# Kernel optimization log

Hardware: AMD Instinct MI355X
Metric: run time of the kernel (lower is better)

Reference implementation:

```python
import jax, jax.numpy as jnp
import numpy as np

N_NODES = 50000
N_EDGES = 800000
NUM_GRAPHS = 128

def _sage_conv(x, src, dst, Wl, b, Wr):
    # PyG SAGEConv: lin_l(mean_{j in N(i)} x_j) + lin_r(x_i); bias only on lin_l
    msgs = x[src]                                             # [E, d] gather
    agg = jax.ops.segment_sum(msgs, dst, num_segments=N_NODES)
    deg = jax.ops.segment_sum(jnp.ones((src.shape[0],), x.dtype), dst,
                              num_segments=N_NODES)
    mean = agg / jnp.maximum(deg, 1.0)[:, None]               # [N, d]
    return mean @ Wl.T + b + x @ Wr.T

def setup_inputs() -> dict:
    key = jax.random.key(0)
    ks = jax.random.split(key, 12)
    d_in, d_h, d_out = 96, 96, 64
    def w(k, o, i):
        return jax.random.normal(k, (o, i), jnp.float32) * (1.0 / np.sqrt(i))
    return {
        "x": jax.random.normal(ks[0], (N_NODES, d_in), jnp.float32),
        "edge_index": jax.random.randint(ks[1], (2, N_EDGES), 0, N_NODES, jnp.int32),
        "batch": jnp.sort(jax.random.randint(ks[2], (N_NODES,), 0, NUM_GRAPHS, jnp.int32)),
        "Wl0": w(ks[3], d_h, d_in), "b0": jnp.zeros((d_h,), jnp.float32), "Wr0": w(ks[4], d_h, d_in),
        "Wl1": w(ks[5], d_h, d_h),  "b1": jnp.zeros((d_h,), jnp.float32), "Wr1": w(ks[6], d_h, d_h),
        "Wl2": w(ks[7], d_out, d_h), "b2": jnp.zeros((d_out,), jnp.float32), "Wr2": w(ks[8], d_out, d_h),
    }

def reference(x, edge_index, batch, Wl0, b0, Wr0, Wl1, b1, Wr1, Wl2, b2, Wr2):
    src, dst = edge_index[0], edge_index[1]
    h = jax.nn.relu(_sage_conv(x, src, dst, Wl0, b0, Wr0))   # dropout: eval mode -> identity
    h = jax.nn.relu(_sage_conv(h, src, dst, Wl1, b1, Wr1))
    h = _sage_conv(h, src, dst, Wl2, b2, Wr2)                 # [N, out]
    # global_mean_pool over graphs
    pooled = jax.ops.segment_sum(h, batch, num_segments=NUM_GRAPHS)
    cnt = jax.ops.segment_sum(jnp.ones((h.shape[0],), h.dtype), batch,
                              num_segments=NUM_GRAPHS)
    return pooled / jnp.maximum(cnt, 1.0)[:, None]            # [num_graphs, out]
```

## Files before the change

kernel.cpp:

```cpp
#include <hip/hip_runtime.h>
#include <stdint.h>
#include <stddef.h>

#define NN 50000
#define NP 50048
#define NE 800000
#define NG 128

#define NBKT 256
#define NPB 196
#define BCAP 4096
#define TILE_E 1536
#define PARTB 521
#define AGB 3125
#define TFB 782

typedef __attribute__((ext_vector_type(8))) short bf16x8;
typedef __attribute__((ext_vector_type(4))) float f32x4;
typedef __attribute__((ext_vector_type(4))) unsigned int u32x4;
typedef unsigned short ushort_t;
typedef unsigned int uint_t;

static __device__ inline ushort_t f2b(float f) {
    union { float f; uint_t u; } v; v.f = f;
    uint_t r = v.u + 0x7FFFu + ((v.u >> 16) & 1u);
    return (ushort_t)(r >> 16);
}
static __device__ inline float blo(uint_t u) {
    union { uint_t u; float f; } v; v.u = u << 16; return v.f;
}
static __device__ inline float bhi(uint_t u) {
    union { uint_t u; float f; } v; v.u = u & 0xFFFF0000u; return v.f;
}

__launch_bounds__(256) static __global__
void part_zero_kernel(const int* __restrict__ src, const int* __restrict__ dst,
                      int* __restrict__ bucket_cnt, uint_t* __restrict__ part,
                      float* __restrict__ out, const int* __restrict__ batch,
                      float* __restrict__ inv_cnt) {
    __shared__ int hist[NBKT];
    int tid = threadIdx.x;
    if (blockIdx.x < PARTB) {
        hist[tid] = 0;
        __syncthreads();
        int base = blockIdx.x * TILE_E;
        int end = min(base + TILE_E, NE);
        for (int i = base + tid; i < end; i += 256)
            atomicAdd(&hist[dst[i] / NPB], 1);
        __syncthreads();
        int r = atomicAdd(&bucket_cnt[tid], hist[tid]);
        __syncthreads();
        hist[tid] = r;
        __syncthreads();
        for (int i = base + tid; i < end; i += 256) {
            int s = src[i], d = dst[i];
            int b = d / NPB;
            int dl = d - b * NPB;
            int p = atomicAdd(&hist[b], 1);
            part[b * BCAP + p] = ((uint_t)dl << 16) | (uint_t)s;
        }
    } else {
        int gid = (blockIdx.x - PARTB) * 256 + tid;
        if (gid < NG * 64) out[gid] = 0.f;
        if (gid < NG) {
            int g = gid;
            int lo = 0, hi = NN;
            while (lo < hi) { int m = (lo + hi) >> 1; if (batch[m] < g) lo = m + 1; else hi = m; }
            int start = lo;
            hi = NN;
            while (lo < hi) { int m = (lo + hi) >> 1; if (batch[m] < g + 1) lo = m + 1; else hi = m; }
            inv_cnt[g] = 1.f / (float)max(lo - start, 1);
        }
    }
}

static __device__ void csr_build_body(int b, char* smem, const uint_t* __restrict__ part,
                                      const int* __restrict__ bucket_cnt,
                                      uint_t* __restrict__ od, ushort_t* __restrict__ csr) {
    uint_t* stage = (uint_t*)smem;
    ushort_t* cstage = (ushort_t*)(smem + 16384);
    int* cnt_s = (int*)(smem + 24576);
    int* scan_l = (int*)(smem + 25600);
    int* cur_l = (int*)(smem + 26624);
    int tid = threadIdx.x;
    int bc = bucket_cnt[tid];
    cnt_s[tid] = bc;
    scan_l[tid] = bc;
    __syncthreads();
    for (int off = 1; off < NBKT; off <<= 1) {
        int t = (tid >= off) ? scan_l[tid - off] : 0;
        __syncthreads();
        scan_l[tid] += t;
        __syncthreads();
    }
    int base = scan_l[b] - cnt_s[b];
    int n = cnt_s[b];
    __syncthreads();
    cnt_s[tid] = 0;
    __syncthreads();
    for (int i = tid; i < n; i += 256) {
        uint_t e = part[(size_t)b * BCAP + i];
        stage[i] = e;
        atomicAdd(&cnt_s[e >> 16], 1);
    }
    __syncthreads();
    int v = cnt_s[tid];
    scan_l[tid] = v;
    __syncthreads();
    for (int off = 1; off < NBKT; off <<= 1) {
        int t = (tid >= off) ? scan_l[tid - off] : 0;
        __syncthreads();
        scan_l[tid] += t;
        __syncthreads();
    }
    int ex = scan_l[tid] - v;
    scan_l[tid] = ex;
    cur_l[tid] = 0;
    __syncthreads();
    int g = b * NPB + tid;
    if (tid < NPB && g < NN) od[g] = ((uint_t)(base + ex) << 8) | (uint_t)v;
    for (int i = tid; i < n; i += 256) {
        uint_t e = stage[i];
        int dl = e >> 16;
        int p = atomicAdd(&cur_l[dl], 1);
        cstage[scan_l[dl] + p] = (ushort_t)(e & 0xFFFFu);
    }
    __syncthreads();
    for (int i = tid; i < n; i += 256) csr[base + i] = cstage[i];
}

template <int DOUT, int NT>
static __device__ void mfma_store(int bid, char* smem, bf16x8 a0, bf16x8 a1, bf16x8 a2,
                                  const float* __restrict__ Wl, const float* __restrict__ bias,
                                  const float* __restrict__ Wr,
                                  ushort_t* __restrict__ tlc, ushort_t* __restrict__ trc) {
    constexpr int DIN = 96;
    short* w_s = (short*)smem;
    int tid = threadIdx.x;
    for (int idx = tid; idx < NT * 3 * 64; idx += 256) {
        int ci = idx >> 6, ln = idx & 63;
        int t = ci / 3, s = ci - 3 * t;
        int o = t * 16 + (ln & 15);
        int c0 = s * 32 + (ln >> 4) * 8;
        const float* wrow = (o < DOUT) ? (Wl + (size_t)o * DIN)
                                       : (Wr + (size_t)(o - DOUT) * DIN);
        float4 v0 = *(const float4*)(wrow + c0);
        float4 v1 = *(const float4*)(wrow + c0 + 4);
        bf16x8 pk;
        pk[0] = (short)f2b(v0.x); pk[1] = (short)f2b(v0.y);
        pk[2] = (short)f2b(v0.z); pk[3] = (short)f2b(v0.w);
        pk[4] = (short)f2b(v1.x); pk[5] = (short)f2b(v1.y);
        pk[6] = (short)f2b(v1.z); pk[7] = (short)f2b(v1.w);
        *(bf16x8*)&w_s[idx * 8] = pk;
    }
    __syncthreads();
    int lane = tid & 63;
    int m0 = bid * 64 + (tid >> 6) * 16;
    const bf16x8* wp = (const bf16x8*)w_s + lane;
    f32x4 acc[NT];
#pragma unroll
    for (int t = 0; t < NT; t++) {
        acc[t] = (f32x4){0.f, 0.f, 0.f, 0.f};
        acc[t] = __builtin_amdgcn_mfma_f32_16x16x32_bf16(a0, wp[(t * 3 + 0) * 64], acc[t], 0, 0, 0);
        acc[t] = __builtin_amdgcn_mfma_f32_16x16x32_bf16(a1, wp[(t * 3 + 1) * 64], acc[t], 0, 0, 0);
        acc[t] = __builtin_amdgcn_mfma_f32_16x16x32_bf16(a2, wp[(t * 3 + 2) * 64], acc[t], 0, 0, 0);
    }
    int quad = lane >> 4, col = lane & 15;
#pragma unroll
    for (int t = 0; t < NT; t++) {
        int o = t * 16 + col;
        bool is_r = (o >= DOUT);
        float bv = is_r ? bias[o - DOUT] : 0.f;
        ushort_t* outp = is_r ? trc : tlc;
        int oo = is_r ? (o - DOUT) : o;
        int cch = oo >> 5, f = oo & 31;
        ushort_t* ob = outp + ((size_t)cch * NN) * 32 + f;
#pragma unroll
        for (int r = 0; r < 4; r++) {
            int node = m0 + quad * 4 + r;
            if (node < NN) ob[(size_t)node * 32] = f2b(acc[t][r] + bv);
        }
    }
}

__launch_bounds__(256) static __global__
void csr_tf0_kernel(const uint_t* __restrict__ part, const int* __restrict__ bucket_cnt,
                    uint_t* __restrict__ od, ushort_t* __restrict__ csr,
                    const float* __restrict__ x, const float* __restrict__ Wl0,
                    const float* __restrict__ b0, const float* __restrict__ Wr0,
                    ushort_t* __restrict__ tlc, ushort_t* __restrict__ trc) {
    __shared__ __align__(16) char smem[36864];
    if (blockIdx.x < NBKT) {
        csr_build_body(blockIdx.x, smem, part, bucket_cnt, od, csr);
    } else {
        int bid = blockIdx.x - NBKT;
        int tid = threadIdx.x;
        int lane = tid & 63;
        int row = bid * 64 + (tid >> 6) * 16 + (lane & 15);
        const float* xr = x + (size_t)min(row, NN - 1) * 96 + (lane >> 4) * 8;
        bf16x8 a0, a1, a2;
#pragma unroll
        for (int s = 0; s < 3; s++) {
            float4 v0 = *(const float4*)(xr + s * 32);
            float4 v1 = *(const float4*)(xr + s * 32 + 4);
            bf16x8 pk;
            pk[0] = (short)f2b(v0.x); pk[1] = (short)f2b(v0.y);
            pk[2] = (short)f2b(v0.z); pk[3] = (short)f2b(v0.w);
            pk[4] = (short)f2b(v1.x); pk[5] = (short)f2b(v1.y);
            pk[6] = (short)f2b(v1.z); pk[7] = (short)f2b(v1.w);
            if (s == 0) a0 = pk; else if (s == 1) a1 = pk; else a2 = pk;
        }
        mfma_store<96, 12>(bid, smem, a0, a1, a2, Wl0, b0, Wr0, tlc, trc);
    }
}

static __device__ inline void gather_accum(const uint_t* __restrict__ tl,
                                           const ushort_t* __restrict__ csr,
                                           int off, int dg, int ng, int fl,
                                           float* __restrict__ acc) {
    int k = 0;
    for (; k + 16 <= dg; k += 16) {
        int s0 = csr[off + k + ng];
        int s1 = csr[off + k + 4 + ng];
        int s2 = csr[off + k + 8 + ng];
        int s3 = csr[off + k + 12 + ng];
        uint4 a0 = *(const uint4*)(tl + (size_t)s0 * 16 + 4 * fl);
        uint4 a1 = *(const uint4*)(tl + (size_t)s1 * 16 + 4 * fl);
        uint4 a2 = *(const uint4*)(tl + (size_t)s2 * 16 + 4 * fl);
        uint4 a3 = *(const uint4*)(tl + (size_t)s3 * 16 + 4 * fl);
        acc[0] += (blo(a0.x) + blo(a1.x)) + (blo(a2.x) + blo(a3.x));
        acc[1] += (bhi(a0.x) + bhi(a1.x)) + (bhi(a2.x) + bhi(a3.x));
        acc[2] += (blo(a0.y) + blo(a1.y)) + (blo(a2.y) + blo(a3.y));
        acc[3] += (bhi(a0.y) + bhi(a1.y)) + (bhi(a2.y) + bhi(a3.y));
        acc[4] += (blo(a0.z) + blo(a1.z)) + (blo(a2.z) + blo(a3.z));
        acc[5] += (bhi(a0.z) + bhi(a1.z)) + (bhi(a2.z) + bhi(a3.z));
        acc[6] += (blo(a0.w) + blo(a1.w)) + (blo(a2.w) + blo(a3.w));
        acc[7] += (bhi(a0.w) + bhi(a1.w)) + (bhi(a2.w) + bhi(a3.w));
    }
    if (k + 8 <= dg) {
        int s0 = csr[off + k + ng];
        int s1 = csr[off + k + 4 + ng];
        uint4 a0 = *(const uint4*)(tl + (size_t)s0 * 16 + 4 * fl);
        uint4 a1 = *(const uint4*)(tl + (size_t)s1 * 16 + 4 * fl);
        acc[0] += blo(a0.x) + blo(a1.x); acc[1] += bhi(a0.x) + bhi(a1.x);
        acc[2] += blo(a0.y) + blo(a1.y); acc[3] += bhi(a0.y) + bhi(a1.y);
        acc[4] += blo(a0.z) + blo(a1.z); acc[5] += bhi(a0.z) + bhi(a1.z);
        acc[6] += blo(a0.w) + blo(a1.w); acc[7] += bhi(a0.w) + bhi(a1.w);
        k += 8;
    }
    if (k + 4 <= dg) {
        int s0 = csr[off + k + ng];
        uint4 a0 = *(const uint4*)(tl + (size_t)s0 * 16 + 4 * fl);
        acc[0] += blo(a0.x); acc[1] += bhi(a0.x);
        acc[2] += blo(a0.y); acc[3] += bhi(a0.y);
        acc[4] += blo(a0.z); acc[5] += bhi(a0.z);
        acc[6] += blo(a0.w); acc[7] += bhi(a0.w);
        k += 4;
    }
    if (ng < dg - k) {
        int s0 = csr[off + k + ng];
        uint4 a0 = *(const uint4*)(tl + (size_t)s0 * 16 + 4 * fl);
        acc[0] += blo(a0.x); acc[1] += bhi(a0.x);
        acc[2] += blo(a0.y); acc[3] += bhi(a0.y);
        acc[4] += blo(a0.z); acc[5] += bhi(a0.z);
        acc[6] += blo(a0.w); acc[7] += bhi(a0.w);
    }
}

template <int DOUT, int NT>
__launch_bounds__(256, 4) static __global__
void aggtf_kernel(const ushort_t* __restrict__ tlin, const ushort_t* __restrict__ trin,
                  const uint_t* __restrict__ od, const ushort_t* __restrict__ csr,
                  const float* __restrict__ Wl, const float* __restrict__ bias,
                  const float* __restrict__ Wr,
                  ushort_t* __restrict__ tlo, ushort_t* __restrict__ tro) {
    constexpr int SMEM = (NT * 3 * 64 * 16 > 12288) ? NT * 3 * 64 * 16 : 12288;
    __shared__ __align__(16) char smem[SMEM];
    uint_t* hbuf = (uint_t*)smem;
    int tid = threadIdx.x;
    int bid = blockIdx.x;
    int lane16 = tid & 15;
    int ng = lane16 >> 2, fl = lane16 & 3;
    for (int c = 0; c < 3; c++) {
        const uint_t* tl = (const uint_t*)tlin + (size_t)c * NN * 16;
        const uint_t* trb = (const uint_t*)trin + (size_t)c * NN * 16;
#pragma unroll
        for (int g = 0; g < 4; g++) {
            int nloc = g * 16 + (tid >> 4);
            int node = bid * 64 + nloc;
            uint_t pd = od[min(node, NN - 1)];
            int off = (int)(pd >> 8);
            int dg = (node < NN) ? (int)(pd & 255u) : 0;
            float acc[8];
#pragma unroll
            for (int q = 0; q < 8; q++) acc[q] = 0.f;
            gather_accum(tl, csr, off, dg, ng, fl, acc);
#pragma unroll
            for (int q = 0; q < 8; q++) {
                acc[q] += __shfl_xor(acc[q], 4, 64);
                acc[q] += __shfl_xor(acc[q], 8, 64);
            }
            float s = 1.f / (float)max(dg, 1);
            u32x4 t = __builtin_nontemporal_load(
                (const u32x4*)(trb + (size_t)min(node, NN - 1) * 16 + 4 * fl));
            if (ng == 0) {
                float v0 = fmaxf(fmaf(acc[0], s, blo(t.x)), 0.f);
                float v1 = fmaxf(fmaf(acc[1], s, bhi(t.x)), 0.f);
                float v2 = fmaxf(fmaf(acc[2], s, blo(t.y)), 0.f);
                float v3 = fmaxf(fmaf(acc[3], s, bhi(t.y)), 0.f);
                float v4 = fmaxf(fmaf(acc[4], s, blo(t.z)), 0.f);
                float v5 = fmaxf(fmaf(acc[5], s, bhi(t.z)), 0.f);
                float v6 = fmaxf(fmaf(acc[6], s, blo(t.w)), 0.f);
                float v7 = fmaxf(fmaf(acc[7], s, bhi(t.w)), 0.f);
                u32x4 o;
                o.x = (uint_t)f2b(v0) | ((uint_t)f2b(v1) << 16);
                o.y = (uint_t)f2b(v2) | ((uint_t)f2b(v3) << 16);
                o.z = (uint_t)f2b(v4) | ((uint_t)f2b(v5) << 16);
                o.w = (uint_t)f2b(v6) | ((uint_t)f2b(v7) << 16);
                *(u32x4*)&hbuf[nloc * 48 + c * 16 + 4 * fl] = o;
            }
        }
    }
    __syncthreads();
    int lane = tid & 63;
    int row = (tid >> 6) * 16 + (lane & 15);
    const ushort_t* hb = (const ushort_t*)smem;
    const ushort_t* hr = hb + row * 96 + (lane >> 4) * 8;
    bf16x8 a0 = *(const bf16x8*)(hr);
    bf16x8 a1 = *(const bf16x8*)(hr + 32);
    bf16x8 a2 = *(const bf16x8*)(hr + 64);
    __syncthreads();
    mfma_store<DOUT, NT>(bid, smem, a0, a1, a2, Wl, bias, Wr, tlo, tro);
}

__launch_bounds__(256) static __global__
void agg_pool_kernel(const ushort_t* __restrict__ tlc, const ushort_t* __restrict__ trc,
                     const uint_t* __restrict__ od, const ushort_t* __restrict__ csr,
                     const int* __restrict__ batch,
                     const float* __restrict__ inv_cnt, float* __restrict__ out) {
    __shared__ float hsum[16][32];
    __shared__ int gids[16];
    int bx = blockIdx.x;
    int c = bx / AGB;
    int b = bx - c * AGB;
    int tid = threadIdx.x;
    int nl = tid >> 4;
    int node = b * 16 + nl;
    int lane = tid & 15;
    int ng = lane >> 2, fl = lane & 3;
    if (tid < 16) gids[tid] = batch[b * 16 + tid];
    const uint_t* tl = (const uint_t*)tlc + (size_t)c * NN * 16;
    uint_t pd = od[node];
    int off = (int)(pd >> 8), dg = (int)(pd & 255u);
    float acc[8];
#pragma unroll
    for (int q = 0; q < 8; q++) acc[q] = 0.f;
    gather_accum(tl, csr, off, dg, ng, fl, acc);
#pragma unroll
    for (int q = 0; q < 8; q++) {
        acc[q] += __shfl_xor(acc[q], 4, 64);
        acc[q] += __shfl_xor(acc[q], 8, 64);
    }
    float s = 1.f / (float)max(dg, 1);
    u32x4 t = __builtin_nontemporal_load(
        (const u32x4*)((const uint_t*)trc + (size_t)c * NN * 16 + (size_t)node * 16 + 4 * fl));
    if (ng == 0) {
        hsum[nl][8 * fl + 0] = fmaf(acc[0], s, blo(t.x));
        hsum[nl][8 * fl + 1] = fmaf(acc[1], s, bhi(t.x));
        hsum[nl][8 * fl + 2] = fmaf(acc[2], s, blo(t.y));
        hsum[nl][8 * fl + 3] = fmaf(acc[3], s, bhi(t.y));
        hsum[nl][8 * fl + 4] = fmaf(acc[4], s, blo(t.z));
        hsum[nl][8 * fl + 5] = fmaf(acc[5], s, bhi(t.z));
        hsum[nl][8 * fl + 6] = fmaf(acc[6], s, blo(t.w));
        hsum[nl][8 * fl + 7] = fmaf(acc[7], s, bhi(t.w));
    }
    __syncthreads();
    if (tid < 32) {
        int gcur = gids[0];
        float ps = 0.f;
        for (int j = 0; j < 16; j++) {
            int g = gids[j];
            if (g != gcur) {
                atomicAdd(&out[gcur * 64 + c * 32 + tid], ps * inv_cnt[gcur]);
                ps = 0.f; gcur = g;
            }
            ps += hsum[j][tid];
        }
        atomicAdd(&out[gcur * 64 + c * 32 + tid], ps * inv_cnt[gcur]);
    }
}

extern "C" void kernel_launch(void* const* d_in, const int* in_sizes, int n_in,
                              void* d_out, int out_size, void* d_ws, size_t ws_size,
                              hipStream_t stream) {
    (void)in_sizes; (void)n_in; (void)out_size; (void)ws_size;
    const float* x   = (const float*)d_in[0];
    const int*   ei  = (const int*)d_in[1];
    const int*   bat = (const int*)d_in[2];
    const float* Wl0 = (const float*)d_in[3];
    const float* b0  = (const float*)d_in[4];
    const float* Wr0 = (const float*)d_in[5];
    const float* Wl1 = (const float*)d_in[6];
    const float* b1  = (const float*)d_in[7];
    const float* Wr1 = (const float*)d_in[8];
    const float* Wl2 = (const float*)d_in[9];
    const float* b2  = (const float*)d_in[10];
    const float* Wr2 = (const float*)d_in[11];
    float* out = (float*)d_out;
    const int* src = ei;
    const int* dst = ei + NE;

    char* p = (char*)d_ws;
    auto carve = [&](size_t bytes) -> char* {
        char* r = p;
        p += (bytes + 255) & ~(size_t)255;
        return r;
    };
    uint_t*   od     = (uint_t*)carve((size_t)NN * 4);
    int*      bucket_cnt = (int*)carve(NBKT * 4);
    float*    inv_cnt = (float*)carve(NG * 4);
    uint_t*   part   = (uint_t*)carve((size_t)NBKT * BCAP * 4);
    ushort_t* csr    = (ushort_t*)carve((size_t)NE * 2);
    ushort_t* tlcA   = (ushort_t*)carve((size_t)3 * NN * 32 * 2);
    ushort_t* trcA   = (ushort_t*)carve((size_t)3 * NN * 32 * 2);
    ushort_t* tlcB   = (ushort_t*)carve((size_t)3 * NN * 32 * 2);
    ushort_t* trcB   = (ushort_t*)carve((size_t)3 * NN * 32 * 2);

    dim3 b256(256);
    hipMemsetAsync(bucket_cnt, 0, NBKT * 4, stream);

    part_zero_kernel<<<dim3(PARTB + 32), b256, 0, stream>>>(src, dst, bucket_cnt, part,
                                                            out, bat, inv_cnt);
    csr_tf0_kernel<<<dim3(NBKT + TFB), b256, 0, stream>>>(part, bucket_cnt, od, csr,
                                                          x, Wl0, b0, Wr0, tlcA, trcA);
    aggtf_kernel<96, 12><<<dim3(TFB), b256, 0, stream>>>(tlcA, trcA, od, csr,
                                                         Wl1, b1, Wr1, tlcB, trcB);
    aggtf_kernel<64, 8><<<dim3(TFB), b256, 0, stream>>>(tlcB, trcB, od, csr,
                                                        Wl2, b2, Wr2, tlcA, trcA);
    agg_pool_kernel<<<dim3(2 * AGB), b256, 0, stream>>>(tlcA, trcA, od, csr, bat,
                                                        inv_cnt, out);
}
```

Before: 288.9 us.

## Pre-pack bf16 weight fragments once and halve aggregation tile per block

Weight matrices for all three layers are converted to bf16 MFMA fragment layout once in the first kernel's spare blocks and stored globally. The transform kernels then read these fragments straight from global/L2 instead of re-converting and staging them into shared memory in every block. The aggregation+transform kernel now handles 32 nodes per block (doubling the grid) and splits output tiles across waves, which cuts shared memory and raises occupancy. The cost is repeated per-wave global loads of the weight fragments and more blocks each redoing CSR offset reads.

```diff
diff --git a/kernel.cpp b/kernel.cpp
--- a/kernel.cpp
+++ b/kernel.cpp
@@ -3,7 +3,6 @@
 #include <stddef.h>
 
 #define NN 50000
-#define NP 50048
 #define NE 800000
 #define NG 128
 
@@ -13,7 +12,12 @@
 #define TILE_E 1536
 #define PARTB 521
 #define AGB 3125
+#define AGB32 1563
 #define TFB 782
+
+#define NF0 2304
+#define NF1 2304
+#define NF2 1536
 
 typedef __attribute__((ext_vector_type(8))) short bf16x8;
 typedef __attribute__((ext_vector_type(4))) float f32x4;
@@ -33,11 +37,36 @@
     union { uint_t u; float f; } v; v.u = u & 0xFFFF0000u; return v.f;
 }
 
+static __device__ inline void pack_frag(int idx, int DOUT,
+                                        const float* __restrict__ Wl,
+                                        const float* __restrict__ Wr,
+                                        ushort_t* __restrict__ wpack) {
+    int ci = idx >> 6, ln = idx & 63;
+    int t = ci / 3, s = ci - 3 * t;
+    int o = t * 16 + (ln & 15);
+    int c0 = s * 32 + (ln >> 4) * 8;
+    const float* wrow = (o < DOUT) ? (Wl + (size_t)o * 96)
+                                   : (Wr + (size_t)(o - DOUT) * 96);
+    float4 v0 = *(const float4*)(wrow + c0);
+    float4 v1 = *(const float4*)(wrow + c0 + 4);
+    bf16x8 pk;
+    pk[0] = (short)f2b(v0.x); pk[1] = (short)f2b(v0.y);
+    pk[2] = (short)f2b(v0.z); pk[3] = (short)f2b(v0.w);
+    pk[4] = (short)f2b(v1.x); pk[5] = (short)f2b(v1.y);
+    pk[6] = (short)f2b(v1.z); pk[7] = (short)f2b(v1.w);
+    *(bf16x8*)&wpack[(size_t)idx * 8] = pk;
+}
+
 __launch_bounds__(256) static __global__
 void part_zero_kernel(const int* __restrict__ src, const int* __restrict__ dst,
                       int* __restrict__ bucket_cnt, uint_t* __restrict__ part,
                       float* __restrict__ out, const int* __restrict__ batch,
-                      float* __restrict__ inv_cnt) {
+                      float* __restrict__ inv_cnt,
+                      const float* __restrict__ Wl0, const float* __restrict__ Wr0,
+                      const float* __restrict__ Wl1, const float* __restrict__ Wr1,
+                      const float* __restrict__ Wl2, const float* __restrict__ Wr2,
+                      ushort_t* __restrict__ wp0, ushort_t* __restrict__ wp1,
+                      ushort_t* __restrict__ wp2) {
     __shared__ int hist[NBKT];
     int tid = threadIdx.x;
     if (blockIdx.x < PARTB) {
@@ -62,6 +91,9 @@
     } else {
         int gid = (blockIdx.x - PARTB) * 256 + tid;
         if (gid < NG * 64) out[gid] = 0.f;
+        if (gid < NF0) pack_frag(gid, 96, Wl0, Wr0, wp0);
+        else if (gid < NF0 + NF1) pack_frag(gid - NF0, 96, Wl1, Wr1, wp1);
+        else if (gid < NF0 + NF1 + NF2) pack_frag(gid - NF0 - NF1, 64, Wl2, Wr2, wp2);
         if (gid < NG) {
             int g = gid;
             int lo = 0, hi = NN;
@@ -129,88 +161,55 @@
     for (int i = tid; i < n; i += 256) csr[base + i] = cstage[i];
 }
 
-template <int DOUT, int NT>
-static __device__ void mfma_store(int bid, char* smem, bf16x8 a0, bf16x8 a1, bf16x8 a2,
-                                  const float* __restrict__ Wl, const float* __restrict__ bias,
-                                  const float* __restrict__ Wr,
-                                  ushort_t* __restrict__ tlc, ushort_t* __restrict__ trc) {
-    constexpr int DIN = 96;
-    short* w_s = (short*)smem;
+__launch_bounds__(256) static __global__
+void csr_tf0_kernel(const uint_t* __restrict__ part, const int* __restrict__ bucket_cnt,
+                    uint_t* __restrict__ od, ushort_t* __restrict__ csr,
+                    const float* __restrict__ x, const ushort_t* __restrict__ wp0,
+                    const float* __restrict__ b0,
+                    ushort_t* __restrict__ tlc, ushort_t* __restrict__ trc) {
+    __shared__ __align__(16) char smem[27648];
+    if (blockIdx.x < NBKT) {
+        csr_build_body(blockIdx.x, smem, part, bucket_cnt, od, csr);
+        return;
+    }
+    int bid = blockIdx.x - NBKT;
     int tid = threadIdx.x;
-    for (int idx = tid; idx < NT * 3 * 64; idx += 256) {
-        int ci = idx >> 6, ln = idx & 63;
-        int t = ci / 3, s = ci - 3 * t;
-        int o = t * 16 + (ln & 15);
-        int c0 = s * 32 + (ln >> 4) * 8;
-        const float* wrow = (o < DOUT) ? (Wl + (size_t)o * DIN)
-                                       : (Wr + (size_t)(o - DOUT) * DIN);
-        float4 v0 = *(const float4*)(wrow + c0);
-        float4 v1 = *(const float4*)(wrow + c0 + 4);
+    int lane = tid & 63;
+    int m0 = bid * 64 + (tid >> 6) * 16;
+    int row = m0 + (lane & 15);
+    const float* xr = x + (size_t)min(row, NN - 1) * 96 + (lane >> 4) * 8;
+    bf16x8 a0, a1, a2;
+#pragma unroll
+    for (int s = 0; s < 3; s++) {
+        float4 v0 = *(const float4*)(xr + s * 32);
+        float4 v1 = *(const float4*)(xr + s * 32 + 4);
         bf16x8 pk;
         pk[0] = (short)f2b(v0.x); pk[1] = (short)f2b(v0.y);
         pk[2] = (short)f2b(v0.z); pk[3] = (short)f2b(v0.w);
         pk[4] = (short)f2b(v1.x); pk[5] = (short)f2b(v1.y);
         pk[6] = (short)f2b(v1.z); pk[7] = (short)f2b(v1.w);
-        *(bf16x8*)&w_s[idx * 8] = pk;
-    }
-    __syncthreads();
-    int lane = tid & 63;
-    int m0 = bid * 64 + (tid >> 6) * 16;
-    const bf16x8* wp = (const bf16x8*)w_s + lane;
-    f32x4 acc[NT];
-#pragma unroll
-    for (int t = 0; t < NT; t++) {
-        acc[t] = (f32x4){0.f, 0.f, 0.f, 0.f};
-        acc[t] = __builtin_amdgcn_mfma_f32_16x16x32_bf16(a0, wp[(t * 3 + 0) * 64], acc[t], 0, 0, 0);
-        acc[t] = __builtin_amdgcn_mfma_f32_16x16x32_bf16(a1, wp[(t * 3 + 1) * 64], acc[t], 0, 0, 0);
-        acc[t] = __builtin_amdgcn_mfma_f32_16x16x32_bf16(a2, wp[(t * 3 + 2) * 64], acc[t], 0, 0, 0);
-    }
+        if (s == 0) a0 = pk; else if (s == 1) a1 = pk; else a2 = pk;
+    }
+    const bf16x8* wp = (const bf16x8*)wp0 + lane;
     int quad = lane >> 4, col = lane & 15;
 #pragma unroll
-    for (int t = 0; t < NT; t++) {
+    for (int t = 0; t < 12; t++) {
+        f32x4 acc = (f32x4){0.f, 0.f, 0.f, 0.f};
+        acc = __builtin_amdgcn_mfma_f32_16x16x32_bf16(a0, wp[(t * 3 + 0) * 64], acc, 0, 0, 0);
+        acc = __builtin_amdgcn_mfma_f32_16x16x32_bf16(a1, wp[(t * 3 + 1) * 64], acc, 0, 0, 0);
+        acc = __builtin_amdgcn_mfma_f32_16x16x32_bf16(a2, wp[(t * 3 + 2) * 64], acc, 0, 0, 0);
         int o = t * 16 + col;
-        bool is_r = (o >= DOUT);
-        float bv = is_r ? bias[o - DOUT] : 0.f;
+        bool is_r = (o >= 96);
+        float bv = is_r ? b0[o - 96] : 0.f;
         ushort_t* outp = is_r ? trc : tlc;
-        int oo = is_r ? (o - DOUT) : o;
+        int oo = is_r ? (o - 96) : o;
         int cch = oo >> 5, f = oo & 31;
         ushort_t* ob = outp + ((size_t)cch * NN) * 32 + f;
 #pragma unroll
         for (int r = 0; r < 4; r++) {
             int node = m0 + quad * 4 + r;
-            if (node < NN) ob[(size_t)node * 32] = f2b(acc[t][r] + bv);
-        }
-    }
-}
-
-__launch_bounds__(256) static __global__
-void csr_tf0_kernel(const uint_t* __restrict__ part, const int* __restrict__ bucket_cnt,
-                    uint_t* __restrict__ od, ushort_t* __restrict__ csr,
-                    const float* __restrict__ x, const float* __restrict__ Wl0,
-                    const float* __restrict__ b0, const float* __restrict__ Wr0,
-                    ushort_t* __restrict__ tlc, ushort_t* __restrict__ trc) {
-    __shared__ __align__(16) char smem[36864];
-    if (blockIdx.x < NBKT) {
-        csr_build_body(blockIdx.x, smem, part, bucket_cnt, od, csr);
-    } else {
-        int bid = blockIdx.x - NBKT;
-        int tid = threadIdx.x;
-        int lane = tid & 63;
-        int row = bid * 64 + (tid >> 6) * 16 + (lane & 15);
-        const float* xr = x + (size_t)min(row, NN - 1) * 96 + (lane >> 4) * 8;
-        bf16x8 a0, a1, a2;
-#pragma unroll
-        for (int s = 0; s < 3; s++) {
-            float4 v0 = *(const float4*)(xr + s * 32);
-            float4 v1 = *(const float4*)(xr + s * 32 + 4);
-            bf16x8 pk;
-            pk[0] = (short)f2b(v0.x); pk[1] = (short)f2b(v0.y);
-            pk[2] = (short)f2b(v0.z); pk[3] = (short)f2b(v0.w);
-            pk[4] = (short)f2b(v1.x); pk[5] = (short)f2b(v1.y);
-            pk[6] = (short)f2b(v1.z); pk[7] = (short)f2b(v1.w);
-            if (s == 0) a0 = pk; else if (s == 1) a1 = pk; else a2 = pk;
-        }
-        mfma_store<96, 12>(bid, smem, a0, a1, a2, Wl0, b0, Wr0, tlc, trc);
+            if (node < NN) ob[(size_t)node * 32] = f2b(acc[r] + bv);
+        }
     }
 }
 
@@ -268,26 +267,23 @@
 }
 
 template <int DOUT, int NT>
-__launch_bounds__(256, 4) static __global__
+__launch_bounds__(256) static __global__
 void aggtf_kernel(const ushort_t* __restrict__ tlin, const ushort_t* __restrict__ trin,
                   const uint_t* __restrict__ od, const ushort_t* __restrict__ csr,
-                  const float* __restrict__ Wl, const float* __restrict__ bias,
-                  const float* __restrict__ Wr,
+                  const ushort_t* __restrict__ wpack, const float* __restrict__ bias,
                   ushort_t* __restrict__ tlo, ushort_t* __restrict__ tro) {
-    constexpr int SMEM = (NT * 3 * 64 * 16 > 12288) ? NT * 3 * 64 * 16 : 12288;
-    __shared__ __align__(16) char smem[SMEM];
-    uint_t* hbuf = (uint_t*)smem;
+    __shared__ __align__(16) uint_t hbuf[32 * 48];
     int tid = threadIdx.x;
     int bid = blockIdx.x;
-    int lane16 = tid & 15;
-    int ng = lane16 >> 2, fl = lane16 & 3;
+    int l16 = tid & 15;
+    int ng = l16 >> 2, fl = l16 & 3;
     for (int c = 0; c < 3; c++) {
         const uint_t* tl = (const uint_t*)tlin + (size_t)c * NN * 16;
         const uint_t* trb = (const uint_t*)trin + (size_t)c * NN * 16;
 #pragma unroll
-        for (int g = 0; g < 4; g++) {
+        for (int g = 0; g < 2; g++) {
             int nloc = g * 16 + (tid >> 4);
-            int node = bid * 64 + nloc;
+            int node = bid * 32 + nloc;
             uint_t pd = od[min(node, NN - 1)];
             int off = (int)(pd >> 8);
             int dg = (node < NN) ? (int)(pd & 255u) : 0;
@@ -322,15 +318,37 @@
         }
     }
     __syncthreads();
-    int lane = tid & 63;
-    int row = (tid >> 6) * 16 + (lane & 15);
-    const ushort_t* hb = (const ushort_t*)smem;
+    int lane = tid & 63, w = tid >> 6;
+    int rt = w & 1, cb = (w >> 1) * (NT / 2);
+    int row = rt * 16 + (lane & 15);
+    const ushort_t* hb = (const ushort_t*)hbuf;
     const ushort_t* hr = hb + row * 96 + (lane >> 4) * 8;
     bf16x8 a0 = *(const bf16x8*)(hr);
     bf16x8 a1 = *(const bf16x8*)(hr + 32);
     bf16x8 a2 = *(const bf16x8*)(hr + 64);
-    __syncthreads();
-    mfma_store<DOUT, NT>(bid, smem, a0, a1, a2, Wl, bias, Wr, tlo, tro);
+    const bf16x8* wp = (const bf16x8*)wpack + lane;
+    int quad = lane >> 4, col = lane & 15;
+    int m0 = bid * 32 + rt * 16;
+#pragma unroll
+    for (int t = 0; t < NT / 2; t++) {
+        int tt = cb + t;
+        f32x4 acc = (f32x4){0.f, 0.f, 0.f, 0.f};
+        acc = __builtin_amdgcn_mfma_f32_16x16x32_bf16(a0, wp[(tt * 3 + 0) * 64], acc, 0, 0, 0);
+        acc = __builtin_amdgcn_mfma_f32_16x16x32_bf16(a1, wp[(tt * 3 + 1) * 64], acc, 0, 0, 0);
+        acc = __builtin_amdgcn_mfma_f32_16x16x32_bf16(a2, wp[(tt * 3 + 2) * 64], acc, 0, 0, 0);
+        int o = tt * 16 + col;
+        bool is_r = (o >= DOUT);
+        float bv = is_r ? bias[o - DOUT] : 0.f;
+        ushort_t* outp = is_r ? tro : tlo;
+        int oo = is_r ? (o - DOUT) : o;
+        int cch = oo >> 5, f = oo & 31;
+        ushort_t* ob = outp + ((size_t)cch * NN) * 32 + f;
+#pragma unroll
+        for (int r = 0; r < 4; r++) {
+            int node = m0 + quad * 4 + r;
+            if (node < NN) ob[(size_t)node * 32] = f2b(acc[r] + bv);
+        }
+    }
 }
 
 __launch_bounds__(256) static __global__
@@ -421,6 +439,9 @@
     float*    inv_cnt = (float*)carve(NG * 4);
     uint_t*   part   = (uint_t*)carve((size_t)NBKT * BCAP * 4);
     ushort_t* csr    = (ushort_t*)carve((size_t)NE * 2);
+    ushort_t* wp0    = (ushort_t*)carve((size_t)NF0 * 16);
+    ushort_t* wp1    = (ushort_t*)carve((size_t)NF1 * 16);
+    ushort_t* wp2    = (ushort_t*)carve((size_t)NF2 * 16);
     ushort_t* tlcA   = (ushort_t*)carve((size_t)3 * NN * 32 * 2);
     ushort_t* trcA   = (ushort_t*)carve((size_t)3 * NN * 32 * 2);
     ushort_t* tlcB   = (ushort_t*)carve((size_t)3 * NN * 32 * 2);
@@ -430,13 +451,15 @@
     hipMemsetAsync(bucket_cnt, 0, NBKT * 4, stream);
 
     part_zero_kernel<<<dim3(PARTB + 32), b256, 0, stream>>>(src, dst, bucket_cnt, part,
-                                                            out, bat, inv_cnt);
+                                                            out, bat, inv_cnt,
+                                                            Wl0, Wr0, Wl1, Wr1, Wl2, Wr2,
+                                                            wp0, wp1, wp2);
     csr_tf0_kernel<<<dim3(NBKT + TFB), b256, 0, stream>>>(part, bucket_cnt, od, csr,
-                                                          x, Wl0, b0, Wr0, tlcA, trcA);
-    aggtf_kernel<96, 12><<<dim3(TFB), b256, 0, stream>>>(tlcA, trcA, od, csr,
-                                                         Wl1, b1, Wr1, tlcB, trcB);
-    aggtf_kernel<64, 8><<<dim3(TFB), b256, 0, stream>>>(tlcB, trcB, od, csr,
-                                                        Wl2, b2, Wr2, tlcA, trcA);
+                                                          x, wp0, b0, tlcA, trcA);
+    aggtf_kernel<96, 12><<<dim3(AGB32), b256, 0, stream>>>(tlcA, trcA, od, csr,
+                                                           wp1, b1, tlcB, trcB);
+    aggtf_kernel<64, 8><<<dim3(AGB32), b256, 0, stream>>>(tlcB, trcB, od, csr,
+                                                          wp2, b2, tlcA, trcA);
     agg_pool_kernel<<<dim3(2 * AGB), b256, 0, stream>>>(tlcA, trcA, od, csr, bat,
                                                         inv_cnt, out);
 }
```

Result: faster. 242.5 us (-16.1%).
